# Performance work log

Hardware: AMD Instinct MI355X
Metric: run time of the kernel (lower is better)

## Reference

```python
import jax, jax.numpy as jnp
import numpy as np

B = 4096
IN_F = 1024
OUT_F = 1024
E = 16
PRIOR_SCALE = 1.0
POSTERIOR_SCALE = 1.0


def _xavier_normal(key, shape):
    # shape = (E, out, in); xavier over (out, in) fan dims
    fan_in, fan_out = shape[2], shape[1]
    std = (2.0 / (fan_in + fan_out)) ** 0.5
    return jax.random.normal(key, shape, dtype=jnp.float32) * std


def setup_inputs() -> dict:
    key = jax.random.key(0)
    k1, k2, k3, k4, k5 = jax.random.split(key, 5)
    logits = jax.random.normal(k1, (B, IN_F), dtype=jnp.float32)
    prior_logits = jax.random.normal(k2, (B, IN_F), dtype=jnp.float32)
    expert_idx = jax.random.randint(k3, (B,), 0, E, dtype=jnp.int32)
    W = _xavier_normal(k4, (E, OUT_F, IN_F))          # base ensemble weights
    b = jnp.zeros((E, OUT_F), dtype=jnp.float32)
    W_prior = _xavier_normal(k5, (E, OUT_F, IN_F))    # frozen prior weights
    b_prior = jnp.zeros((E, OUT_F), dtype=jnp.float32)
    return {"logits": logits, "prior_logits": prior_logits, "W": W, "b": b,
            "W_prior": W_prior, "b_prior": b_prior, "expert_idx": expert_idx}


def reference(logits, prior_logits, W, b, W_prior, b_prior, expert_idx):
    # One-hot per-sample expert routing. Faithful to the torch per-sample
    # branch: out[i] = Linear_{e_i}(logits[i]), blended with frozen prior.
    onehot = jax.nn.one_hot(expert_idx, E, dtype=logits.dtype)       # [B,E]
    y_all = jnp.einsum('bi,eoi->beo', logits, W) + b                  # [B,E,O]
    y = jnp.einsum('be,beo->bo', onehot, y_all)                       # [B,O]
    yp_all = jnp.einsum('bi,eoi->beo', prior_logits, W_prior) + b_prior
    yp = jnp.einsum('be,beo->bo', onehot, yp_all)
    out = POSTERIOR_SCALE * y + PRIOR_SCALE * yp
    return out[:, None, :]                                            # [B,1,O]
```

## Files before the change

### kernel.cpp

```cpp
#include <hip/hip_runtime.h>
#include <hip/hip_bf16.h>

typedef __bf16 bf16x8 __attribute__((ext_vector_type(8)));
typedef float f32x4 __attribute__((ext_vector_type(4)));

constexpr int NE   = 16;
constexpr int NB   = 4096;
constexpr int INF  = 1024;
constexpr int OUTF = 1024;
constexpr int BM = 64, BN = 128, BK = 64;
constexpr int NSTEP  = INF / BK;
constexpr int ABYTES = BM * BK * 2;
constexpr int BBYTES = BN * BK * 2;
constexpr int MAXMT  = NB / BM;

__device__ __forceinline__ unsigned short f2bf(float f) {
  union { float f; unsigned int u; } x{f};
  unsigned int r = x.u + 0x7fffu + ((x.u >> 16) & 1u);
  return (unsigned short)(r >> 16);
}

__global__ void route_init_kernel(int* counts) {
  if (threadIdx.x < NE) counts[threadIdx.x] = 0;
}

__global__ void route_kernel(const int* __restrict__ eidx, int* counts, int* rows) {
  int i = blockIdx.x * blockDim.x + threadIdx.x;
  if (i < NB) {
    int e = eidx[i];
    int slot = atomicAdd(&counts[e], 1);
    rows[e * NB + slot] = i;
  }
}

__global__ __launch_bounds__(256, 3) void ens_gemm_kernel(
    const float* __restrict__ X0,
    const float* __restrict__ X1,
    const float* __restrict__ W0,
    const float* __restrict__ B0,
    const float* __restrict__ W1,
    const float* __restrict__ B1,
    const int* __restrict__ counts,
    const int* __restrict__ rows,
    float* __restrict__ out)
{
  const int e  = blockIdx.z >> 1;
  const int kh = blockIdx.z & 1;
  const int mt = blockIdx.y;
  const int n0 = blockIdx.x * BN;
  const int me = counts[e];
  const int m0 = mt * BM;
  if (m0 >= me) return;

  __shared__ __align__(16) char smem[2 * (ABYTES + BBYTES)];
  __shared__ int rid[BM];

  const int t = threadIdx.x;
  if (t < BM) {
    int slot = m0 + t;
    rid[t] = (slot < me) ? rows[e * NB + slot] : -1;
  }
  __syncthreads();

  const int tr = t >> 4;
  const int tc = t & 15;
  const int w  = t >> 6;
  const int l  = t & 63;
  const int wm = (w >> 1) * 32;
  const int wn = (w & 1) * 64;
  const int lr = l & 15;
  const int lk = l >> 4;

  const float* xs = kh ? X1 : X0;
  const float* ws = (kh ? W1 : W0) + (size_t)e * OUTF * INF;

  int rcache[4];
#pragma unroll
  for (int p = 0; p < 4; ++p) rcache[p] = rid[p * 16 + tr];

  f32x4 acc[2][4] = {};

  float4 ra[4], rw[8];

  auto gload = [&](int s) {
    const int kc = s * BK + tc * 4;
#pragma unroll
    for (int p = 0; p < 4; ++p) {
      const int r = rcache[p];
      if (r >= 0) ra[p] = *(const float4*)(xs + (size_t)r * INF + kc);
      else        ra[p] = make_float4(0.f, 0.f, 0.f, 0.f);
    }
#pragma unroll
    for (int p = 0; p < 8; ++p) {
      const int row = p * 16 + tr;
      rw[p] = *(const float4*)(ws + (size_t)(n0 + row) * INF + kc);
    }
  };

  auto swrite = [&](int buf) {
    char* ab = smem + buf * (ABYTES + BBYTES);
    char* bb = ab + ABYTES;
    const int c0 = tc * 8;
#pragma unroll
    for (int p = 0; p < 4; ++p) {
      const int row = p * 16 + tr;
      const int off = row * (BK * 2) + (c0 ^ ((row & 7) << 4));
      ushort4 ha;
      ha.x = f2bf(ra[p].x); ha.y = f2bf(ra[p].y);
      ha.z = f2bf(ra[p].z); ha.w = f2bf(ra[p].w);
      *(ushort4*)(ab + off) = ha;
    }
#pragma unroll
    for (int p = 0; p < 8; ++p) {
      const int row = p * 16 + tr;
      const int off = row * (BK * 2) + (c0 ^ ((row & 7) << 4));
      ushort4 hw;
      hw.x = f2bf(rw[p].x); hw.y = f2bf(rw[p].y);
      hw.z = f2bf(rw[p].z); hw.w = f2bf(rw[p].w);
      *(ushort4*)(bb + off) = hw;
    }
  };

  auto compute = [&](int buf) {
    const char* ab = smem + buf * (ABYTES + BBYTES);
    const char* bb = ab + ABYTES;
#pragma unroll
    for (int kk = 0; kk < 2; ++kk) {
      const int kb = kk * 64 + lk * 16;
      bf16x8 af[2], bv[4];
#pragma unroll
      for (int f = 0; f < 2; ++f) {
        const int arow = wm + f * 16 + lr;
        af[f] = *(const bf16x8*)(ab + arow * (BK * 2) + (kb ^ ((arow & 7) << 4)));
      }
#pragma unroll
      for (int f = 0; f < 4; ++f) {
        const int brow = wn + f * 16 + lr;
        bv[f] = *(const bf16x8*)(bb + brow * (BK * 2) + (kb ^ ((brow & 7) << 4)));
      }
#pragma unroll
      for (int fm = 0; fm < 2; ++fm)
#pragma unroll
        for (int fn = 0; fn < 4; ++fn)
          acc[fm][fn] = __builtin_amdgcn_mfma_f32_16x16x32_bf16(
              af[fm], bv[fn], acc[fm][fn], 0, 0, 0);
    }
  };

  gload(0);
  swrite(0);
  __syncthreads();

  int cur = 0;
  for (int s = 0; s < NSTEP; ++s) {
    if (s + 1 < NSTEP) gload(s + 1);
    compute(cur);
    if (s + 1 < NSTEP) swrite(cur ^ 1);
    __syncthreads();
    cur ^= 1;
  }

  const float* Bb0 = B0 + e * OUTF;
  const float* Bb1 = B1 + e * OUTF;
#pragma unroll
  for (int fn = 0; fn < 4; ++fn) {
    const int gcol = n0 + wn + fn * 16 + lr;
    const float bias = (kh == 0) ? (Bb0[gcol] + Bb1[gcol]) : 0.f;
#pragma unroll
    for (int fm = 0; fm < 2; ++fm) {
#pragma unroll
      for (int j = 0; j < 4; ++j) {
        const int sl = wm + fm * 16 + lk * 4 + j;
        const int r = rid[sl];
        if (r >= 0) atomicAdd(&out[(size_t)r * OUTF + gcol], acc[fm][fn][j] + bias);
      }
    }
  }
}

extern "C" void kernel_launch(void* const* d_in, const int* in_sizes, int n_in,
                              void* d_out, int out_size, void* d_ws, size_t ws_size,
                              hipStream_t stream) {
  const float* logits = (const float*)d_in[0];
  const float* prior  = (const float*)d_in[1];
  const float* W      = (const float*)d_in[2];
  const float* b      = (const float*)d_in[3];
  const float* Wp     = (const float*)d_in[4];
  const float* bp     = (const float*)d_in[5];
  const int*   eidx   = (const int*)d_in[6];
  float* out = (float*)d_out;

  int* counts = (int*)d_ws;
  int* rows   = counts + 32;

  hipMemsetAsync(d_out, 0, (size_t)out_size * sizeof(float), stream);

  hipLaunchKernelGGL(route_init_kernel, dim3(1), dim3(64), 0, stream, counts);
  hipLaunchKernelGGL(route_kernel, dim3(NB / 256), dim3(256), 0, stream,
                     eidx, counts, rows);

  dim3 grid(OUTF / BN, MAXMT, NE * 2);
  hipLaunchKernelGGL(ens_gemm_kernel, grid, dim3(256), 0, stream,
                     logits, prior, W, b, Wp, bp, counts, rows, out);
}
```

Baseline: 104.6 us.

## Launch a compacted per-expert tile list and use native bf16 conversion

A new single-wave kernel prefix-sums the per-expert tile counts and writes a compact list of (expert, m-tile) descriptors. The GEMM grid then covers only those tiles instead of every possible m-tile for every expert, so most of the mostly empty, early-exiting workgroups are no longer launched. The hand-written round-to-nearest float-to-bf16 bit manipulation is also replaced by compiler bf16 casts, which can map to packed hardware conversion instructions. The cost is one extra tiny kernel launch in the serial chain before the GEMM.

```diff
diff --git a/kernel.cpp b/kernel.cpp
--- a/kernel.cpp
+++ b/kernel.cpp
@@ -12,16 +12,17 @@
 constexpr int NSTEP  = INF / BK;
 constexpr int ABYTES = BM * BK * 2;
 constexpr int BBYTES = BN * BK * 2;
-constexpr int MAXMT  = NB / BM;
-
-__device__ __forceinline__ unsigned short f2bf(float f) {
-  union { float f; unsigned int u; } x{f};
-  unsigned int r = x.u + 0x7fffu + ((x.u >> 16) & 1u);
-  return (unsigned short)(r >> 16);
-}
-
-__global__ void route_init_kernel(int* counts) {
-  if (threadIdx.x < NE) counts[threadIdx.x] = 0;
+constexpr int MAXT   = NB / BM + NE - 1;
+
+__device__ __forceinline__ uint2 cvt4(const float4 v) {
+  union { __bf16 h[4]; uint2 u; } r;
+  r.h[0] = (__bf16)v.x; r.h[1] = (__bf16)v.y;
+  r.h[2] = (__bf16)v.z; r.h[3] = (__bf16)v.w;
+  return r.u;
+}
+
+__global__ void route_init_kernel(int* ws) {
+  if (threadIdx.x < 32) ws[threadIdx.x] = 0;
 }
 
 __global__ void route_kernel(const int* __restrict__ eidx, int* counts, int* rows) {
@@ -30,6 +31,23 @@
     int e = eidx[i];
     int slot = atomicAdd(&counts[e], 1);
     rows[e * NB + slot] = i;
+  }
+}
+
+__global__ void tile_kernel(int* ws) {
+  int lane = threadIdx.x;
+  int nt = 0;
+  if (lane < NE) nt = (ws[lane] + BM - 1) / BM;
+  int pre = nt;
+  for (int d = 1; d < NE; d <<= 1) {
+    int v = __shfl_up(pre, d);
+    if (lane >= d && lane < NE) pre += v;
+  }
+  int total = __shfl(pre, NE - 1);
+  if (lane == 0) ws[16] = total;
+  if (lane < NE) {
+    int base = pre - nt;
+    for (int m = 0; m < nt; ++m) ws[32 + base + m] = (lane << 16) | m;
   }
 }
 
@@ -40,17 +58,18 @@
     const float* __restrict__ B0,
     const float* __restrict__ W1,
     const float* __restrict__ B1,
-    const int* __restrict__ counts,
+    const int* __restrict__ ws_i,
     const int* __restrict__ rows,
     float* __restrict__ out)
 {
-  const int e  = blockIdx.z >> 1;
-  const int kh = blockIdx.z & 1;
-  const int mt = blockIdx.y;
+  const int nt = ws_i[16];
+  if (blockIdx.y >= nt) return;
+  const int desc = ws_i[32 + blockIdx.y];
+  const int e  = desc >> 16;
+  const int m0 = (desc & 0xffff) * BM;
+  const int kh = blockIdx.z;
   const int n0 = blockIdx.x * BN;
-  const int me = counts[e];
-  const int m0 = mt * BM;
-  if (m0 >= me) return;
+  const int me = ws_i[e];
 
   __shared__ __align__(16) char smem[2 * (ABYTES + BBYTES)];
   __shared__ int rid[BM];
@@ -72,7 +91,7 @@
   const int lk = l >> 4;
 
   const float* xs = kh ? X1 : X0;
-  const float* ws = (kh ? W1 : W0) + (size_t)e * OUTF * INF;
+  const float* wsp = (kh ? W1 : W0) + (size_t)e * OUTF * INF;
 
   int rcache[4];
 #pragma unroll
@@ -87,14 +106,12 @@
 #pragma unroll
     for (int p = 0; p < 4; ++p) {
       const int r = rcache[p];
-      if (r >= 0) ra[p] = *(const float4*)(xs + (size_t)r * INF + kc);
-      else        ra[p] = make_float4(0.f, 0.f, 0.f, 0.f);
-    }
-#pragma unroll
-    for (int p = 0; p < 8; ++p) {
-      const int row = p * 16 + tr;
-      rw[p] = *(const float4*)(ws + (size_t)(n0 + row) * INF + kc);
-    }
+      ra[p] = (r >= 0) ? *(const float4*)(xs + (size_t)r * INF + kc)
+                       : make_float4(0.f, 0.f, 0.f, 0.f);
+    }
+#pragma unroll
+    for (int p = 0; p < 8; ++p)
+      rw[p] = *(const float4*)(wsp + (size_t)(n0 + p * 16 + tr) * INF + kc);
   };
 
   auto swrite = [&](int buf) {
@@ -104,20 +121,12 @@
 #pragma unroll
     for (int p = 0; p < 4; ++p) {
       const int row = p * 16 + tr;
-      const int off = row * (BK * 2) + (c0 ^ ((row & 7) << 4));
-      ushort4 ha;
-      ha.x = f2bf(ra[p].x); ha.y = f2bf(ra[p].y);
-      ha.z = f2bf(ra[p].z); ha.w = f2bf(ra[p].w);
-      *(ushort4*)(ab + off) = ha;
+      *(uint2*)(ab + row * (BK * 2) + (c0 ^ ((row & 7) << 4))) = cvt4(ra[p]);
     }
 #pragma unroll
     for (int p = 0; p < 8; ++p) {
       const int row = p * 16 + tr;
-      const int off = row * (BK * 2) + (c0 ^ ((row & 7) << 4));
-      ushort4 hw;
-      hw.x = f2bf(rw[p].x); hw.y = f2bf(rw[p].y);
-      hw.z = f2bf(rw[p].z); hw.w = f2bf(rw[p].w);
-      *(ushort4*)(bb + off) = hw;
+      *(uint2*)(bb + row * (BK * 2) + (c0 ^ ((row & 7) << 4))) = cvt4(rw[p]);
     }
   };
 
@@ -190,16 +199,17 @@
   const int*   eidx   = (const int*)d_in[6];
   float* out = (float*)d_out;
 
-  int* counts = (int*)d_ws;
-  int* rows   = counts + 32;
-
-  hipMemsetAsync(d_out, 0, (size_t)out_size * sizeof(float), stream);
-
-  hipLaunchKernelGGL(route_init_kernel, dim3(1), dim3(64), 0, stream, counts);
+  int* wsi  = (int*)d_ws;
+  int* rows = wsi + 128;
+
+  (void)hipMemsetAsync(d_out, 0, (size_t)out_size * sizeof(float), stream);
+
+  hipLaunchKernelGGL(route_init_kernel, dim3(1), dim3(64), 0, stream, wsi);
   hipLaunchKernelGGL(route_kernel, dim3(NB / 256), dim3(256), 0, stream,
-                     eidx, counts, rows);
-
-  dim3 grid(OUTF / BN, MAXMT, NE * 2);
+                     eidx, wsi, rows);
+  hipLaunchKernelGGL(tile_kernel, dim3(1), dim3(64), 0, stream, wsi);
+
+  dim3 grid(OUTF / BN, MAXT, 2);
   hipLaunchKernelGGL(ens_gemm_kernel, grid, dim3(256), 0, stream,
-                     logits, prior, W, b, Wp, bp, counts, rows, out);
-}
+                     logits, prior, W, b, Wp, bp, wsi, rows, out);
+}
```

Result: slower. 128.9 us (+23.2%).
